# Performance work log

Measured on AMD Instinct MI355X. Metric: run time of the kernel, lower is better.

The kernel has to match this reference:

```python
import jax, jax.numpy as jnp
import numpy as np

B, S, E, H, R = 512, 50, 128, 8, 32
D = E // H  # depth per head
USERS, ITEMS, ALLSEQ, NCLASS = 50000, 20000, 20000, 5


def setup_inputs() -> dict:
    key = jax.random.key(0)
    ks = jax.random.split(key, 20)
    n = lambda k, shp, s=0.05: jax.random.normal(k, shp, dtype=jnp.float32) * s
    return {
        "user": jax.random.randint(ks[0], (B,), 0, USERS),
        "item": jax.random.randint(ks[1], (B,), 0, ITEMS),
        "neighbor": jax.random.randint(ks[2], (B, S), 0, USERS),
        "seq": jax.random.randint(ks[3], (B, S), 0, ALLSEQ),
        "user_emb_table": n(ks[4], (USERS, E)),
        "item_emb_table": n(ks[5], (ITEMS, E)),
        "user_item_LCU": n(ks[6], (ALLSEQ, R, E), 0.01),
        "item_user_LCU": n(ks[7], (ALLSEQ, R, E), 0.01),
        "wq": n(ks[8], (E, E)), "bq": jnp.zeros((E,), jnp.float32),
        "wk": n(ks[9], (E, E)), "bk": jnp.zeros((E,), jnp.float32),
        "wv": n(ks[10], (E, E)), "bv": jnp.zeros((E,), jnp.float32),
        "wo": n(ks[11], (E, E)), "bo": jnp.zeros((E,), jnp.float32),
        "fc_w": n(ks[12], (R, NCLASS)), "fc_b": jnp.zeros((NCLASS,), jnp.float32),
    }


def _forward(user, item, neighbor, seq,
             user_emb_table, item_emb_table, user_item_LCU, item_user_LCU,
             wq, bq, wk, bk, wv, bv, wo, bo, fc_w, fc_b):
    user_emb = user_emb_table[user]            # [B,E]
    neighbor_emb = user_emb_table[neighbor]    # [B,S,E]
    item_emb = item_emb_table[item]            # [B,E]
    weight = (neighbor > 0).astype(jnp.float32)  # [B,S] padding mask (1=real)

    # ---- single-query multi-head attention (use_attention=True) ----
    q = (user_emb @ wq + bq).reshape(B, H, D)                       # [B,H,D]
    k = (neighbor_emb @ wk + bk).reshape(B, S, H, D).transpose(0, 2, 1, 3)  # [B,H,S,D]
    v = (neighbor_emb @ wv + bv).reshape(B, S, H, D).transpose(0, 2, 1, 3)  # [B,H,S,D]
    logits = jnp.einsum('bhd,bhsd->bhs', q, k) / jnp.sqrt(jnp.float32(D))
    logits = logits + (1.0 - weight)[:, None, :] * (-1e9)           # mask padding
    attn = jax.nn.softmax(logits, axis=-1)                          # [B,H,S]
    ctx = attn[..., None] * v                                       # [B,H,S,D]
    ctx = ctx.transpose(0, 2, 1, 3).reshape(B, S, E)                # [B,S,E]
    neighbor_emb = ctx @ wo + bo                                    # [B,S,E]

    # ---- region embedding ----
    K_ui = user_item_LCU[seq]   # [B,S,R,E]
    K_iu = item_user_LCU[seq]   # [B,S,R,E]
    neighbor_profile = jnp.einsum('bsre,bse->bsr', K_iu, neighbor_emb)  # [B,S,R]
    item_profile = jnp.einsum('bsre,be->bsr', K_ui, item_emb)          # [B,S,R]
    neighbor_rating = neighbor_profile * item_profile * weight[:, :, None]
    user_rating_vector = jnp.max(neighbor_rating, axis=1)              # [B,R]

    # ---- rating classifier ----
    return jax.nn.softmax(user_rating_vector @ fc_w + fc_b, axis=-1)   # [B,NCLASS]


def reference(user, item, neighbor, seq,
              user_emb_table, item_emb_table, user_item_LCU, item_user_LCU,
              wq, bq, wk, bk, wv, bv, wo, bo, fc_w, fc_b):
    return _forward(user, item, neighbor, seq,
                    user_emb_table, item_emb_table, user_item_LCU, item_user_LCU,
                    wq, bq, wk, bk, wv, bv, wo, bo, fc_w, fc_b)
```

## Files before the change

kernel.cpp:

```cpp
#include <hip/hip_runtime.h>
#include <hip/hip_bf16.h>
#include <math.h>

#define BB 512
#define SS 50
#define EE 128
#define HH 8
#define RR 32
#define NC 5

__device__ __forceinline__ void fma4(float4& a, float s, const float4& w) {
    a.x = fmaf(s, w.x, a.x);
    a.y = fmaf(s, w.y, a.y);
    a.z = fmaf(s, w.z, a.z);
    a.w = fmaf(s, w.w, a.w);
}

__device__ __forceinline__ float dot4(const float4& a, const float4& b) {
    return a.x*b.x + a.y*b.y + a.z*b.z + a.w*b.w;
}

__global__ __launch_bounds__(256) void attn_kernel(
    const int* __restrict__ user, const int* __restrict__ item,
    const int* __restrict__ neighbor,
    const float* __restrict__ uet, const float* __restrict__ iet,
    const float* __restrict__ wq, const float* __restrict__ bq,
    const float* __restrict__ wk, const float* __restrict__ bk,
    const float* __restrict__ wv, const float* __restrict__ bv,
    const float* __restrict__ wo, const float* __restrict__ bo,
    float* __restrict__ ws_item, float* __restrict__ ws_ne2)
{
    __shared__ float ne[SS][EE];
    __shared__ float vbuf[SS][EE];
    __shared__ float ue[EE];
    __shared__ float qs[EE];
    __shared__ float attn_s[HH][SS];
    __shared__ float maskadd[SS];

    const int b = blockIdx.x;
    const int t = threadIdx.x;

    if (t < EE) {
        ue[t] = uet[(size_t)user[b]*EE + t];
    } else {
        ws_item[(size_t)b*EE + (t - EE)] = iet[(size_t)item[b]*EE + (t - EE)];
    }
    for (int idx = t; idx < SS*(EE/4); idx += 256) {
        int s = idx >> 5, c = idx & 31;
        const float4* src = (const float4*)(uet + (size_t)neighbor[b*SS + s]*EE);
        ((float4*)&ne[s][0])[c] = src[c];
    }
    if (t < SS) maskadd[t] = (neighbor[b*SS + t] > 0) ? 0.f : -1e9f;
    __syncthreads();

    if (t < EE) {
        float acc = bq[t];
        #pragma unroll 4
        for (int e = 0; e < EE; ++e) acc = fmaf(ue[e], wq[e*EE + t], acc);
        qs[t] = acc;
    }
    __syncthreads();

    {
        const int m  = t >> 7;
        const int r  = t & 127;
        const int cg = r & 31;
        const int sg = r >> 5;
        const float4* w4p = (const float4*)(m ? wv : wk);

        float4 acc[13];
        #pragma unroll
        for (int i = 0; i < 13; ++i) acc[i] = make_float4(0.f,0.f,0.f,0.f);

        for (int e4 = 0; e4 < EE/4; ++e4) {
            float4 w0 = w4p[(e4*4 + 0)*(EE/4) + cg];
            float4 w1 = w4p[(e4*4 + 1)*(EE/4) + cg];
            float4 w2 = w4p[(e4*4 + 2)*(EE/4) + cg];
            float4 w3 = w4p[(e4*4 + 3)*(EE/4) + cg];
            #pragma unroll
            for (int i = 0; i < 13; ++i) {
                int s = i*4 + sg;
                if (s < SS) {
                    float4 nv = ((const float4*)&ne[s][0])[e4];
                    fma4(acc[i], nv.x, w0);
                    fma4(acc[i], nv.y, w1);
                    fma4(acc[i], nv.z, w2);
                    fma4(acc[i], nv.w, w3);
                }
            }
        }

        if (m == 0) {
            float4 q4  = ((const float4*)qs)[cg];
            float4 bk4 = ((const float4*)bk)[cg];
            #pragma unroll
            for (int i = 0; i < 13; ++i) {
                int s = i*4 + sg;
                if (s < SS) {
                    float4 kk;
                    kk.x = acc[i].x + bk4.x; kk.y = acc[i].y + bk4.y;
                    kk.z = acc[i].z + bk4.z; kk.w = acc[i].w + bk4.w;
                    float p = dot4(kk, q4);
                    p += __shfl_xor(p, 1);
                    p += __shfl_xor(p, 2);
                    if ((cg & 3) == 0) attn_s[cg >> 2][s] = p * 0.25f + maskadd[s];
                }
            }
        } else {
            float4 bv4 = ((const float4*)bv)[cg];
            #pragma unroll
            for (int i = 0; i < 13; ++i) {
                int s = i*4 + sg;
                if (s < SS) {
                    float4 vv;
                    vv.x = acc[i].x + bv4.x; vv.y = acc[i].y + bv4.y;
                    vv.z = acc[i].z + bv4.z; vv.w = acc[i].w + bv4.w;
                    ((float4*)&vbuf[s][0])[cg] = vv;
                }
            }
        }
    }
    __syncthreads();

    if (t < 64) {
        int h = t >> 3, l = t & 7;
        float mx = -3e38f;
        #pragma unroll
        for (int i = 0; i < 7; ++i) { int s = i*8 + l; if (s < SS) mx = fmaxf(mx, attn_s[h][s]); }
        mx = fmaxf(mx, __shfl_xor(mx, 1));
        mx = fmaxf(mx, __shfl_xor(mx, 2));
        mx = fmaxf(mx, __shfl_xor(mx, 4));
        float ev[7]; float sm = 0.f;
        #pragma unroll
        for (int i = 0; i < 7; ++i) {
            int s = i*8 + l; ev[i] = 0.f;
            if (s < SS) { ev[i] = expf(attn_s[h][s] - mx); sm += ev[i]; }
        }
        sm += __shfl_xor(sm, 1);
        sm += __shfl_xor(sm, 2);
        sm += __shfl_xor(sm, 4);
        float inv = 1.f / sm;
        #pragma unroll
        for (int i = 0; i < 7; ++i) { int s = i*8 + l; if (s < SS) attn_s[h][s] = ev[i] * inv; }
    }
    __syncthreads();

    for (int idx = t; idx < SS*(EE/4); idx += 256) {
        int s = idx >> 5, c = idx & 31;
        int h = c >> 2;
        float a = attn_s[h][s];
        float4 vv = ((float4*)&vbuf[s][0])[c];
        vv.x *= a; vv.y *= a; vv.z *= a; vv.w *= a;
        ((float4*)&vbuf[s][0])[c] = vv;
    }
    __syncthreads();

    {
        const int cg = t & 31;
        const int sg = t >> 5;
        const float4* w4p = (const float4*)wo;
        float4 acc[7];
        #pragma unroll
        for (int i = 0; i < 7; ++i) acc[i] = make_float4(0.f,0.f,0.f,0.f);

        for (int e4 = 0; e4 < EE/4; ++e4) {
            float4 w0 = w4p[(e4*4 + 0)*(EE/4) + cg];
            float4 w1 = w4p[(e4*4 + 1)*(EE/4) + cg];
            float4 w2 = w4p[(e4*4 + 2)*(EE/4) + cg];
            float4 w3 = w4p[(e4*4 + 3)*(EE/4) + cg];
            #pragma unroll
            for (int i = 0; i < 7; ++i) {
                int s = i*8 + sg;
                if (s < SS) {
                    float4 nv = ((const float4*)&vbuf[s][0])[e4];
                    fma4(acc[i], nv.x, w0);
                    fma4(acc[i], nv.y, w1);
                    fma4(acc[i], nv.z, w2);
                    fma4(acc[i], nv.w, w3);
                }
            }
        }
        float4 bo4 = ((const float4*)bo)[cg];
        #pragma unroll
        for (int i = 0; i < 7; ++i) {
            int s = i*8 + sg;
            if (s < SS) {
                float4 o;
                o.x = acc[i].x + bo4.x; o.y = acc[i].y + bo4.y;
                o.z = acc[i].z + bo4.z; o.w = acc[i].w + bo4.w;
                ((float4*)ws_ne2)[((size_t)b*SS + s)*(EE/4) + cg] = o;
            }
        }
    }
}

__global__ __launch_bounds__(256) void region_kernel(
    const int* __restrict__ neighbor, const int* __restrict__ seq,
    const float* __restrict__ ui_lcu, const float* __restrict__ iu_lcu,
    const float* __restrict__ ws_item, const float* __restrict__ ws_ne2,
    float* __restrict__ ws_rating)
{
    __shared__ float ner[EE], ier[EE];
    const int bs = blockIdx.x;
    const int b  = bs / SS;
    const int t  = threadIdx.x;

    if (t < EE) ner[t] = ws_ne2[(size_t)bs*EE + t];
    else        ier[t - EE] = ws_item[(size_t)b*EE + (t - EE)];

    const int nb = neighbor[bs];
    const int j  = seq[bs];
    const float w = (nb > 0) ? 1.f : 0.f;
    __syncthreads();

    const int r = t >> 3, l = t & 7;
    const float4* kiu = (const float4*)(iu_lcu + ((size_t)j*RR + r)*EE);
    const float4* kui = (const float4*)(ui_lcu + ((size_t)j*RR + r)*EE);
    const float4* n4 = (const float4*)ner;
    const float4* i4 = (const float4*)ier;

    float np_ = 0.f, ip_ = 0.f;
    #pragma unroll
    for (int i = 0; i < 4; ++i) {
        int c = l + 8*i;
        float4 a = kiu[c];
        float4 x = n4[c];
        np_ += dot4(a, x);
        float4 g = kui[c];
        float4 y = i4[c];
        ip_ += dot4(g, y);
    }
    np_ += __shfl_xor(np_, 1); np_ += __shfl_xor(np_, 2); np_ += __shfl_xor(np_, 4);
    ip_ += __shfl_xor(ip_, 1); ip_ += __shfl_xor(ip_, 2); ip_ += __shfl_xor(ip_, 4);

    if (l == 0) ws_rating[(size_t)bs*RR + r] = np_ * ip_ * w;
}

__global__ __launch_bounds__(64) void head_kernel(
    const float* __restrict__ ws_rating,
    const float* __restrict__ fc_w, const float* __restrict__ fc_b,
    float* __restrict__ out)
{
    __shared__ float urv[RR];
    __shared__ float lg[NC];
    const int b = blockIdx.x, t = threadIdx.x;

    if (t < RR) {
        float m = -3e38f;
        const float* p = ws_rating + (size_t)b*SS*RR + t;
        for (int s = 0; s < SS; ++s) m = fmaxf(m, p[s*RR]);
        urv[t] = m;
    }
    __syncthreads();
    if (t < NC) {
        float acc = fc_b[t];
        #pragma unroll
        for (int r = 0; r < RR; ++r) acc = fmaf(urv[r], fc_w[r*NC + t], acc);
        lg[t] = acc;
    }
    __syncthreads();
    if (t < NC) {
        float mx = lg[0];
        #pragma unroll
        for (int c = 1; c < NC; ++c) mx = fmaxf(mx, lg[c]);
        float sm = 0.f;
        #pragma unroll
        for (int c = 0; c < NC; ++c) sm += expf(lg[c] - mx);
        out[b*NC + t] = expf(lg[t] - mx) / sm;
    }
}

extern "C" void kernel_launch(void* const* d_in, const int* in_sizes, int n_in,
                              void* d_out, int out_size, void* d_ws, size_t ws_size,
                              hipStream_t stream) {
    const int*   user     = (const int*)d_in[0];
    const int*   item     = (const int*)d_in[1];
    const int*   neighbor = (const int*)d_in[2];
    const int*   seq      = (const int*)d_in[3];
    const float* uet      = (const float*)d_in[4];
    const float* iet      = (const float*)d_in[5];
    const float* ui_lcu   = (const float*)d_in[6];
    const float* iu_lcu   = (const float*)d_in[7];
    const float* wq = (const float*)d_in[8];   const float* bq = (const float*)d_in[9];
    const float* wk = (const float*)d_in[10];  const float* bk = (const float*)d_in[11];
    const float* wv = (const float*)d_in[12];  const float* bv = (const float*)d_in[13];
    const float* wo = (const float*)d_in[14];  const float* bo = (const float*)d_in[15];
    const float* fcw = (const float*)d_in[16]; const float* fcb = (const float*)d_in[17];

    float* ws = (float*)d_ws;
    float* ws_item   = ws;
    float* ws_ne2    = ws_item + (size_t)BB*EE;
    float* ws_rating = ws_ne2  + (size_t)BB*SS*EE;
    float* out = (float*)d_out;

    hipLaunchKernelGGL(attn_kernel, dim3(BB), dim3(256), 0, stream,
                       user, item, neighbor, uet, iet,
                       wq, bq, wk, bk, wv, bv, wo, bo, ws_item, ws_ne2);
    hipLaunchKernelGGL(region_kernel, dim3(BB*SS), dim3(256), 0, stream,
                       neighbor, seq, ui_lcu, iu_lcu, ws_item, ws_ne2, ws_rating);
    hipLaunchKernelGGL(head_kernel, dim3(BB), dim3(64), 0, stream,
                       ws_rating, fcw, fcb, out);
}
```

Before: 201.6 us.

## Sort region work by seq index and split item profile into attention launch

Builds a counting-sort permutation of the (b,s) pairs by seq id using histogram, scan and scatter kernels. Region blocks then run in that order so that pairs sharing the same 16 KB LCU slab run close together and can reuse it from cache. The item-profile dot products run as extra blocks inside the attention launch, overlapping LCU reads with the attention compute, and the neighbor profile becomes its own pass. In exchange it adds four small launches including a single-block scan, atomics, and an extra workspace round trip for the item-profile values.

```diff
diff --git a/kernel.cpp b/kernel.cpp
--- a/kernel.cpp
+++ b/kernel.cpp
@@ -8,6 +8,8 @@
 #define HH 8
 #define RR 32
 #define NC 5
+#define NSEQ 20000
+#define NBS (BB*SS)
 
 __device__ __forceinline__ void fma4(float4& a, float s, const float4& w) {
     a.x = fmaf(s, w.x, a.x);
@@ -20,31 +22,118 @@
     return a.x*b.x + a.y*b.y + a.z*b.z + a.w*b.w;
 }
 
-__global__ __launch_bounds__(256) void attn_kernel(
+__global__ __launch_bounds__(256) void hist_kernel(const int* __restrict__ seq,
+                                                   int* __restrict__ hist) {
+    int i = blockIdx.x * 256 + threadIdx.x;
+    if (i < NBS) atomicAdd(&hist[seq[i]], 1);
+}
+
+__global__ __launch_bounds__(1024) void scan_kernel(int* __restrict__ hist) {
+    const int t = threadIdx.x;
+    const int CH = 20;
+    const int base = t * CH;
+    int loc[CH];
+    int s = 0;
+    #pragma unroll
+    for (int i = 0; i < CH; ++i) {
+        int idx = base + i;
+        int v = (idx < NSEQ) ? hist[idx] : 0;
+        loc[i] = s; s += v;
+    }
+    const int lane = t & 63, w = t >> 6;
+    int incl = s;
+    #pragma unroll
+    for (int off = 1; off < 64; off <<= 1) {
+        int n = __shfl_up(incl, off);
+        if (lane >= off) incl += n;
+    }
+    __shared__ int wsum[16];
+    if (lane == 63) wsum[w] = incl;
+    __syncthreads();
+    if (t == 0) {
+        int acc = 0;
+        #pragma unroll
+        for (int k = 0; k < 16; ++k) { int v = wsum[k]; wsum[k] = acc; acc += v; }
+    }
+    __syncthreads();
+    const int excl = incl - s + wsum[w];
+    #pragma unroll
+    for (int i = 0; i < CH; ++i) {
+        int idx = base + i;
+        if (idx < NSEQ) hist[idx] = excl + loc[i];
+    }
+}
+
+__global__ __launch_bounds__(256) void scatter_kernel(const int* __restrict__ seq,
+                                                      int* __restrict__ hist,
+                                                      int* __restrict__ perm) {
+    int i = blockIdx.x * 256 + threadIdx.x;
+    if (i < NBS) {
+        int pos = atomicAdd(&hist[seq[i]], 1);
+        perm[pos] = i;
+    }
+}
+
+union SMemU {
+    struct {
+        float ne[SS][EE];
+        float vbuf[SS][EE];
+        float ue[EE];
+        float qs[EE];
+        float attn[HH][SS];
+        float maskadd[SS];
+    } a;
+    struct {
+        float ier[EE];
+    } r;
+};
+
+__global__ __launch_bounds__(256) void attn_item_kernel(
     const int* __restrict__ user, const int* __restrict__ item,
-    const int* __restrict__ neighbor,
+    const int* __restrict__ neighbor, const int* __restrict__ seq,
     const float* __restrict__ uet, const float* __restrict__ iet,
+    const float* __restrict__ ui_lcu,
     const float* __restrict__ wq, const float* __restrict__ bq,
     const float* __restrict__ wk, const float* __restrict__ bk,
     const float* __restrict__ wv, const float* __restrict__ bv,
     const float* __restrict__ wo, const float* __restrict__ bo,
-    float* __restrict__ ws_item, float* __restrict__ ws_ne2)
+    const int* __restrict__ perm,
+    float* __restrict__ ws_ne2, float* __restrict__ ws_ip)
 {
-    __shared__ float ne[SS][EE];
-    __shared__ float vbuf[SS][EE];
-    __shared__ float ue[EE];
-    __shared__ float qs[EE];
-    __shared__ float attn_s[HH][SS];
-    __shared__ float maskadd[SS];
+    __shared__ SMemU sm;
+    const int t = threadIdx.x;
+
+    if (blockIdx.x >= BB) {
+        const int bs = perm[blockIdx.x - BB];
+        const int b  = bs / SS;
+        const int j  = seq[bs];
+        if (t < EE) sm.r.ier[t] = iet[(size_t)item[b]*EE + t];
+        __syncthreads();
+
+        const int r = t >> 3, l = t & 7;
+        const float4* kui = (const float4*)(ui_lcu + ((size_t)j*RR + r)*EE);
+        const float4* i4  = (const float4*)sm.r.ier;
+        float ip_ = 0.f;
+        #pragma unroll
+        for (int i = 0; i < 4; ++i) {
+            int c = l + 8*i;
+            ip_ += dot4(kui[c], i4[c]);
+        }
+        ip_ += __shfl_xor(ip_, 1); ip_ += __shfl_xor(ip_, 2); ip_ += __shfl_xor(ip_, 4);
+        if (l == 0) ws_ip[(size_t)bs*RR + r] = ip_;
+        return;
+    }
+
+    float (*ne)[EE]   = sm.a.ne;
+    float (*vbuf)[EE] = sm.a.vbuf;
+    float* ue = sm.a.ue;
+    float* qs = sm.a.qs;
+    float (*attn_s)[SS] = sm.a.attn;
+    float* maskadd = sm.a.maskadd;
 
     const int b = blockIdx.x;
-    const int t = threadIdx.x;
-
-    if (t < EE) {
-        ue[t] = uet[(size_t)user[b]*EE + t];
-    } else {
-        ws_item[(size_t)b*EE + (t - EE)] = iet[(size_t)item[b]*EE + (t - EE)];
-    }
+
+    if (t < EE) ue[t] = uet[(size_t)user[b]*EE + t];
     for (int idx = t; idx < SS*(EE/4); idx += 256) {
         int s = idx >> 5, c = idx & 31;
         const float4* src = (const float4*)(uet + (size_t)neighbor[b*SS + s]*EE);
@@ -130,16 +219,16 @@
         mx = fmaxf(mx, __shfl_xor(mx, 1));
         mx = fmaxf(mx, __shfl_xor(mx, 2));
         mx = fmaxf(mx, __shfl_xor(mx, 4));
-        float ev[7]; float sm = 0.f;
+        float ev[7]; float sm_ = 0.f;
         #pragma unroll
         for (int i = 0; i < 7; ++i) {
             int s = i*8 + l; ev[i] = 0.f;
-            if (s < SS) { ev[i] = expf(attn_s[h][s] - mx); sm += ev[i]; }
-        }
-        sm += __shfl_xor(sm, 1);
-        sm += __shfl_xor(sm, 2);
-        sm += __shfl_xor(sm, 4);
-        float inv = 1.f / sm;
+            if (s < SS) { ev[i] = expf(attn_s[h][s] - mx); sm_ += ev[i]; }
+        }
+        sm_ += __shfl_xor(sm_, 1);
+        sm_ += __shfl_xor(sm_, 2);
+        sm_ += __shfl_xor(sm_, 4);
+        float inv = 1.f / sm_;
         #pragma unroll
         for (int i = 0; i < 7; ++i) { int s = i*8 + l; if (s < SS) attn_s[h][s] = ev[i] * inv; }
     }
@@ -194,46 +283,35 @@
     }
 }
 
-__global__ __launch_bounds__(256) void region_kernel(
+__global__ __launch_bounds__(256) void neighbor_kernel(
     const int* __restrict__ neighbor, const int* __restrict__ seq,
-    const float* __restrict__ ui_lcu, const float* __restrict__ iu_lcu,
-    const float* __restrict__ ws_item, const float* __restrict__ ws_ne2,
+    const float* __restrict__ iu_lcu,
+    const float* __restrict__ ws_ne2, const float* __restrict__ ws_ip,
+    const int* __restrict__ perm,
     float* __restrict__ ws_rating)
 {
-    __shared__ float ner[EE], ier[EE];
-    const int bs = blockIdx.x;
-    const int b  = bs / SS;
+    __shared__ float ner[EE];
+    const int bs = perm[blockIdx.x];
     const int t  = threadIdx.x;
 
     if (t < EE) ner[t] = ws_ne2[(size_t)bs*EE + t];
-    else        ier[t - EE] = ws_item[(size_t)b*EE + (t - EE)];
-
-    const int nb = neighbor[bs];
-    const int j  = seq[bs];
-    const float w = (nb > 0) ? 1.f : 0.f;
+    const int j = seq[bs];
+    const float w = (neighbor[bs] > 0) ? 1.f : 0.f;
     __syncthreads();
 
     const int r = t >> 3, l = t & 7;
     const float4* kiu = (const float4*)(iu_lcu + ((size_t)j*RR + r)*EE);
-    const float4* kui = (const float4*)(ui_lcu + ((size_t)j*RR + r)*EE);
     const float4* n4 = (const float4*)ner;
-    const float4* i4 = (const float4*)ier;
-
-    float np_ = 0.f, ip_ = 0.f;
+
+    float np_ = 0.f;
     #pragma unroll
     for (int i = 0; i < 4; ++i) {
         int c = l + 8*i;
-        float4 a = kiu[c];
-        float4 x = n4[c];
-        np_ += dot4(a, x);
-        float4 g = kui[c];
-        float4 y = i4[c];
-        ip_ += dot4(g, y);
+        np_ += dot4(kiu[c], n4[c]);
     }
     np_ += __shfl_xor(np_, 1); np_ += __shfl_xor(np_, 2); np_ += __shfl_xor(np_, 4);
-    ip_ += __shfl_xor(ip_, 1); ip_ += __shfl_xor(ip_, 2); ip_ += __shfl_xor(ip_, 4);
-
-    if (l == 0) ws_rating[(size_t)bs*RR + r] = np_ * ip_ * w;
+
+    if (l == 0) ws_rating[(size_t)bs*RR + r] = np_ * ws_ip[(size_t)bs*RR + r] * w;
 }
 
 __global__ __launch_bounds__(64) void head_kernel(
@@ -288,16 +366,25 @@
     const float* fcw = (const float*)d_in[16]; const float* fcb = (const float*)d_in[17];
 
     float* ws = (float*)d_ws;
-    float* ws_item   = ws;
-    float* ws_ne2    = ws_item + (size_t)BB*EE;
-    float* ws_rating = ws_ne2  + (size_t)BB*SS*EE;
+    float* ws_ne2    = ws;
+    float* ws_ip     = ws_ne2    + (size_t)BB*SS*EE;
+    float* ws_rating = ws_ip     + (size_t)BB*SS*RR;
+    int*   hist      = (int*)(ws_rating + (size_t)BB*SS*RR);
+    int*   perm      = hist + NSEQ;
     float* out = (float*)d_out;
 
-    hipLaunchKernelGGL(attn_kernel, dim3(BB), dim3(256), 0, stream,
-                       user, item, neighbor, uet, iet,
-                       wq, bq, wk, bk, wv, bv, wo, bo, ws_item, ws_ne2);
-    hipLaunchKernelGGL(region_kernel, dim3(BB*SS), dim3(256), 0, stream,
-                       neighbor, seq, ui_lcu, iu_lcu, ws_item, ws_ne2, ws_rating);
+    hipMemsetAsync(hist, 0, NSEQ * sizeof(int), stream);
+    hipLaunchKernelGGL(hist_kernel, dim3((NBS + 255)/256), dim3(256), 0, stream, seq, hist);
+    hipLaunchKernelGGL(scan_kernel, dim3(1), dim3(1024), 0, stream, hist);
+    hipLaunchKernelGGL(scatter_kernel, dim3((NBS + 255)/256), dim3(256), 0, stream, seq, hist, perm);
+
+    hipLaunchKernelGGL(attn_item_kernel, dim3(BB + NBS), dim3(256), 0, stream,
+                       user, item, neighbor, seq, uet, iet, ui_lcu,
+                       wq, bq, wk, bk, wv, bv, wo, bo, perm, ws_ne2, ws_ip);
+
+    hipLaunchKernelGGL(neighbor_kernel, dim3(NBS), dim3(256), 0, stream,
+                       neighbor, seq, iu_lcu, ws_ne2, ws_ip, perm, ws_rating);
+
     hipLaunchKernelGGL(head_kernel, dim3(BB), dim3(64), 0, stream,
                        ws_rating, fcw, fcb, out);
 }
```

New measurement: 267.5 us. +32.7%, slower.
